# Kernel optimization log

Hardware: AMD Instinct MI355X
Metric: run time of the kernel (lower is better)

Reference implementation:

```python
import jax, jax.numpy as jnp
import numpy as np

NUM_GROUPS = 19  # cityscapes classes; groups in the grouped conv
GATES = 4
SLABS = 4  # hidden slabs per class


def setup_inputs() -> dict:
    key = jax.random.key(0)
    k1, k2, k3, k4, k5 = jax.random.split(key, 5)
    B, H, Wd = 4, 256, 512
    x = jax.random.normal(k1, (B, NUM_GROUPS, H, Wd), dtype=jnp.float32)
    h = jax.random.normal(k2, (B, NUM_GROUPS, SLABS, H, Wd), dtype=jnp.float32)
    c = jax.random.normal(k3, (B, NUM_GROUPS, SLABS, H, Wd), dtype=jnp.float32)
    # Conv2d(95 -> 304, k=3, groups=19): weight (304, 5, 3, 3), bias (304,)
    fan_in = 5 * 3 * 3
    bound = 1.0 / np.sqrt(fan_in)
    W = jax.random.uniform(k4, (4 * NUM_GROUPS * SLABS, 5, 3, 3), minval=-bound, maxval=bound, dtype=jnp.float32)
    b = jax.random.uniform(k5, (4 * NUM_GROUPS * SLABS,), minval=-bound, maxval=bound, dtype=jnp.float32)
    return {"x": x, "h": h, "c": c, "W": W, "b": b}


def reference(x, h, c, W, b):
    B, _, H, Wd = x.shape
    # Strided interleave: channel g*5+0 = x[:,g], g*5+1..4 = h[:,g,0..3]
    xh = jnp.concatenate([x[:, :, None], h], axis=2).reshape(B, NUM_GROUPS * 5, H, Wd)
    A = jax.lax.conv_general_dilated(
        xh, W, window_strides=(1, 1), padding=[(1, 1), (1, 1)],
        feature_group_count=NUM_GROUPS,
        dimension_numbers=("NCHW", "OIHW", "NCHW"))
    A = A + b[None, :, None, None]
    A = A.reshape(B, NUM_GROUPS, GATES, SLABS, H, Wd)
    i = jax.nn.sigmoid(A[:, :, 0])
    f = jax.nn.sigmoid(A[:, :, 1])
    o = jax.nn.sigmoid(A[:, :, 2])
    g = jnp.tanh(A[:, :, 3])
    new_c = f * c + i * g
    new_h = o * jnp.tanh(new_c)
    return (new_h, new_c)
```

## Files before the change

### kernel.cpp

```cpp
#include <hip/hip_runtime.h>
#include <hip/hip_bf16.h>

#define NG      19
#define HEIGHT  256
#define WIDTH   512
#define HW      (HEIGHT*WIDTH)
#define BATCH   4
#define TH      16
#define TW      64
#define HALO_R  18
#define HALO_CU 34
#define CH_U32  (HALO_R*HALO_CU)
#define LDS_U32 (5*CH_U32)
#define WFRAG_SHORTS (NG*64*16)
#define BIAS_FLOATS (NG*16)

typedef __attribute__((ext_vector_type(8))) short short8;
typedef __attribute__((ext_vector_type(4))) float f32x4;
typedef __attribute__((ext_vector_type(4))) unsigned int u32x4;

static __device__ __forceinline__ unsigned int bfbits(float f) {
    return (unsigned int)__builtin_bit_cast(unsigned short, __float2bfloat16(f));
}
static __device__ __forceinline__ unsigned int fsh16(unsigned int hi, unsigned int lo) {
    return (unsigned int)((((unsigned long long)hi << 32) | lo) >> 16);
}
__device__ __forceinline__ float fsigmoid(float x) {
    return __builtin_amdgcn_rcpf(1.0f + __builtin_amdgcn_exp2f(-1.44269504f * x));
}
__device__ __forceinline__ float ftanh(float x) {
    return 2.0f * __builtin_amdgcn_rcpf(1.0f + __builtin_amdgcn_exp2f(-2.88539008f * x)) - 1.0f;
}

__global__ void wxform_kernel(const float* __restrict__ W,
                              const float* __restrict__ b,
                              short* __restrict__ wdst,
                              float* __restrict__ bdst) {
    int i = blockIdx.x * 256 + threadIdx.x;
    if (i < WFRAG_SHORTS) {
        int g   = i / 1024;
        int r   = i & 1023;
        int l   = r >> 4;
        int j   = r & 15;
        int q   = l >> 4;
        int row = l & 15;
        int s    = row >> 2;
        int gate = row & 3;
        int half = j >> 3;
        int jj   = j & 7;
        int m  = 8*half + 2*q + (jj >> 2);
        int kc = jj & 3;
        float wv = 0.0f;
        if (m <= 14 && kc < 3) {
            int ic = m / 3, kr = m % 3;
            int oc = g*16 + gate*4 + s;
            wv = W[((oc*5 + ic)*3 + kr)*3 + kc];
        }
        wdst[i] = (short)__builtin_bit_cast(unsigned short, __float2bfloat16(wv));
    } else if (i < WFRAG_SHORTS + BIAS_FLOATS) {
        int idx = i - WFRAG_SHORTS;
        int g = idx >> 4;
        int r = idx & 15;
        int s = r >> 2, gate = r & 3;
        bdst[idx] = b[g*16 + gate*4 + s];
    }
}

__launch_bounds__(256, 4)
__global__ void convlstm_mfma(const float* __restrict__ x,
                              const float* __restrict__ h,
                              const float* __restrict__ c,
                              const short* __restrict__ wfrag,
                              const float* __restrict__ biasp,
                              float* __restrict__ out) {
    __shared__ unsigned int lds[LDS_U32];

    const int t    = threadIdx.x;
    const int bid  = blockIdx.x;
    const int bg   = bid >> 7;
    const int tile = bid & 127;
    const int tr0  = (tile >> 3) * TH;
    const int tc0  = (tile & 7)  * TW;
    const int g    = bg % NG;

    const int w  = t >> 6;
    const int l  = t & 63;
    const int q  = l >> 4;
    const int li = l & 15;

    const int NC_OFF   = BATCH * NG * 4 * HW;
    const int rowbase0 = (bg*4 + q)*HW + (tr0 + w*4)*WIDTH + tc0 + 4*li;
    f32x4 cp[4];
    #pragma unroll
    for (int tr4 = 0; tr4 < 4; ++tr4)
        cp[tr4] = __builtin_nontemporal_load(
            reinterpret_cast<const f32x4*>(c + rowbase0 + tr4*WIDTH));

    const short8* ap = reinterpret_cast<const short8*>(wfrag + (g*64 + l)*16);
    const short8 a_lo = ap[0];
    const short8 a_hi = ap[1];
    f32x4 bias4;
    {
        float4 bv = *reinterpret_cast<const float4*>(biasp + g*16 + q*4);
        bias4[0] = bv.x; bias4[1] = bv.y; bias4[2] = bv.z; bias4[3] = bv.w;
    }

    const float* xb = x + bg * HW;
    const float* hb = h + (bg * 4) * HW;
    for (int p = t; p < LDS_U32; p += 256) {
        int ch  = p / CH_U32;  int rem = p - ch * CH_U32;
        int r   = rem / HALO_CU;
        int j   = rem - r * HALO_CU;
        int gr  = tr0 + r - 1;
        int gc  = tc0 + 2*j - 1;
        const float* base = (ch == 0) ? xb : hb + (ch - 1) * HW;
        float v0 = 0.0f, v1 = 0.0f;
        if (gr >= 0 && gr < HEIGHT) {
            const float* rowp = base + gr * WIDTH;
            if (gc >= 0 && gc < WIDTH) v0 = rowp[gc];
            if (gc + 1 < WIDTH)        v1 = rowp[gc + 1];
        }
        lds[p] = bfbits(v0) | (bfbits(v1) << 16);
    }
    __syncthreads();

    int cbase[4];
    #pragma unroll
    for (int i = 0; i < 4; ++i) {
        int m = (i < 2) ? (2*q + i) : (8 + 2*q + (i - 2));
        if (m > 14) m = 14;
        cbase[i] = (m/3)*(CH_U32*4) + (m%3)*(HALO_CU*4) + 8*li;
    }
    const char* ldsb = reinterpret_cast<const char*>(lds);

    #pragma unroll
    for (int tr4 = 0; tr4 < 4; ++tr4) {
        const int tr = w*4 + tr4;
        uint2 dv[4][2];
        #pragma unroll
        for (int i = 0; i < 4; ++i) {
            const uint2* pp = reinterpret_cast<const uint2*>(
                ldsb + cbase[i] + tr * (HALO_CU*4));
            dv[i][0] = pp[0];
            dv[i][1] = pp[1];
        }
        float nh4[4], nc4[4];
        #pragma unroll
        for (int n = 0; n < 4; ++n) {
            u32x4 blo_u, bhi_u;
            #pragma unroll
            for (int i = 0; i < 4; ++i) {
                const unsigned int d0 = dv[i][0].x, d1 = dv[i][0].y;
                const unsigned int d2 = dv[i][1].x, d3 = dv[i][1].y;
                unsigned int w0, w1;
                if (n == 0)      { w0 = d0;           w1 = d1;           }
                else if (n == 1) { w0 = fsh16(d1,d0); w1 = fsh16(d2,d1); }
                else if (n == 2) { w0 = d1;           w1 = d2;           }
                else             { w0 = fsh16(d2,d1); w1 = fsh16(d3,d2); }
                if (i < 2) { blo_u[2*i]     = w0; blo_u[2*i+1]     = w1; }
                else       { bhi_u[2*(i-2)] = w0; bhi_u[2*(i-2)+1] = w1; }
            }
            const short8 blo = __builtin_bit_cast(short8, blo_u);
            const short8 bhi = __builtin_bit_cast(short8, bhi_u);

            f32x4 acc = bias4;
            acc = __builtin_amdgcn_mfma_f32_16x16x32_bf16(a_lo, blo, acc, 0, 0, 0);
            acc = __builtin_amdgcn_mfma_f32_16x16x32_bf16(a_hi, bhi, acc, 0, 0, 0);

            const float cv = cp[tr4][n];
            const float iv = fsigmoid(acc[0]);
            const float fv = fsigmoid(acc[1]);
            const float ov = fsigmoid(acc[2]);
            const float gv = ftanh   (acc[3]);
            const float nc = fv * cv + iv * gv;
            nc4[n] = nc;
            nh4[n] = ov * ftanh(nc);
        }
        const int rowchan = rowbase0 + tr4*WIDTH;
        f32x4 nhv; nhv[0]=nh4[0]; nhv[1]=nh4[1]; nhv[2]=nh4[2]; nhv[3]=nh4[3];
        f32x4 ncv; ncv[0]=nc4[0]; ncv[1]=nc4[1]; ncv[2]=nc4[2]; ncv[3]=nc4[3];
        __builtin_nontemporal_store(nhv, reinterpret_cast<f32x4*>(out + rowchan));
        __builtin_nontemporal_store(ncv, reinterpret_cast<f32x4*>(out + NC_OFF + rowchan));
    }
}

extern "C" void kernel_launch(void* const* d_in, const int* in_sizes, int n_in,
                              void* d_out, int out_size, void* d_ws, size_t ws_size,
                              hipStream_t stream) {
    (void)in_sizes; (void)n_in; (void)out_size; (void)ws_size;
    const float* x = (const float*)d_in[0];
    const float* h = (const float*)d_in[1];
    const float* c = (const float*)d_in[2];
    const float* W = (const float*)d_in[3];
    const float* b = (const float*)d_in[4];
    float* out = (float*)d_out;

    short* wdst = (short*)d_ws;
    float* bdst = (float*)((char*)d_ws + WFRAG_SHORTS * sizeof(short));

    hipLaunchKernelGGL(wxform_kernel,
                       dim3((WFRAG_SHORTS + BIAS_FLOATS + 255) / 256), dim3(256),
                       0, stream, W, b, wdst, bdst);
    hipLaunchKernelGGL(convlstm_mfma, dim3(BATCH * NG * 128), dim3(256),
                       0, stream, x, h, c, (const short*)wdst, bdst, out);
}
```

Before: 146.5 us.

## Fold gate scales into weights, dual-shifted LDS layout, vectorized halo loads, merged reciprocals

Prescales the weights and bias by -log2(e) (or -2log2(e) for the g gate) so that the gate nonlinearities become bare exp2 calls. The sigmoid and tanh reciprocals are then merged algebraically into two rcp operations per output. The halo fill now issues vectorized float2 global loads and stores two LDS copies offset by one bf16 element, which removes the 16-bit funnel shifts in the inner loop. The c loads are also software-pipelined one row ahead. In exchange, LDS use doubles, which may lower occupancy, and the merged reciprocals slightly change numerical behavior for large exponents.

```diff
diff --git a/kernel.cpp b/kernel.cpp
--- a/kernel.cpp
+++ b/kernel.cpp
@@ -12,24 +12,21 @@
 #define HALO_CU 34
 #define CH_U32  (HALO_R*HALO_CU)
 #define LDS_U32 (5*CH_U32)
+#define ROWB    (HALO_CU*4)
+#define CHB     (CH_U32*4)
 #define WFRAG_SHORTS (NG*64*16)
-#define BIAS_FLOATS (NG*16)
+#define BIAS_FLOATS  (NG*16)
 
 typedef __attribute__((ext_vector_type(8))) short short8;
 typedef __attribute__((ext_vector_type(4))) float f32x4;
+typedef __attribute__((ext_vector_type(2))) float f32x2;
 typedef __attribute__((ext_vector_type(4))) unsigned int u32x4;
 
 static __device__ __forceinline__ unsigned int bfbits(float f) {
     return (unsigned int)__builtin_bit_cast(unsigned short, __float2bfloat16(f));
 }
-static __device__ __forceinline__ unsigned int fsh16(unsigned int hi, unsigned int lo) {
-    return (unsigned int)((((unsigned long long)hi << 32) | lo) >> 16);
-}
-__device__ __forceinline__ float fsigmoid(float x) {
-    return __builtin_amdgcn_rcpf(1.0f + __builtin_amdgcn_exp2f(-1.44269504f * x));
-}
-__device__ __forceinline__ float ftanh(float x) {
-    return 2.0f * __builtin_amdgcn_rcpf(1.0f + __builtin_amdgcn_exp2f(-2.88539008f * x)) - 1.0f;
+static __device__ __forceinline__ unsigned int pack2(float lo, float hi) {
+    return bfbits(lo) | (bfbits(hi) << 16);
 }
 
 __global__ void wxform_kernel(const float* __restrict__ W,
@@ -54,7 +51,8 @@
         if (m <= 14 && kc < 3) {
             int ic = m / 3, kr = m % 3;
             int oc = g*16 + gate*4 + s;
-            wv = W[((oc*5 + ic)*3 + kr)*3 + kc];
+            float scale = (gate == 3) ? -2.88539008f : -1.44269504f;
+            wv = scale * W[((oc*5 + ic)*3 + kr)*3 + kc];
         }
         wdst[i] = (short)__builtin_bit_cast(unsigned short, __float2bfloat16(wv));
     } else if (i < WFRAG_SHORTS + BIAS_FLOATS) {
@@ -62,7 +60,8 @@
         int g = idx >> 4;
         int r = idx & 15;
         int s = r >> 2, gate = r & 3;
-        bdst[idx] = b[g*16 + gate*4 + s];
+        float scale = (gate == 3) ? -2.88539008f : -1.44269504f;
+        bdst[idx] = scale * b[g*16 + gate*4 + s];
     }
 }
 
@@ -73,15 +72,16 @@
                               const short* __restrict__ wfrag,
                               const float* __restrict__ biasp,
                               float* __restrict__ out) {
-    __shared__ unsigned int lds[LDS_U32];
-
-    const int t    = threadIdx.x;
-    const int bid  = blockIdx.x;
-    const int bg   = bid >> 7;
-    const int tile = bid & 127;
-    const int tr0  = (tile >> 3) * TH;
-    const int tc0  = (tile & 7)  * TW;
-    const int g    = bg % NG;
+    __shared__ unsigned int lds0[LDS_U32];
+    __shared__ unsigned int lds1[LDS_U32];
+
+    const int t     = threadIdx.x;
+    const int bid   = blockIdx.x;
+    const int plane = bid >> 7;
+    const int tile  = bid & 127;
+    const int tr0   = (tile >> 3) * TH;
+    const int tc0   = (tile & 7)  * TW;
+    const int g     = plane % NG;
 
     const int w  = t >> 6;
     const int l  = t & 63;
@@ -89,76 +89,95 @@
     const int li = l & 15;
 
     const int NC_OFF   = BATCH * NG * 4 * HW;
-    const int rowbase0 = (bg*4 + q)*HW + (tr0 + w*4)*WIDTH + tc0 + 4*li;
-    f32x4 cp[4];
-    #pragma unroll
-    for (int tr4 = 0; tr4 < 4; ++tr4)
-        cp[tr4] = __builtin_nontemporal_load(
-            reinterpret_cast<const f32x4*>(c + rowbase0 + tr4*WIDTH));
+    const int rowbase0 = (plane*4 + q)*HW + (tr0 + w*4)*WIDTH + tc0 + 4*li;
+
+    f32x4 cvrow = __builtin_nontemporal_load(
+        reinterpret_cast<const f32x4*>(c + rowbase0));
 
     const short8* ap = reinterpret_cast<const short8*>(wfrag + (g*64 + l)*16);
     const short8 a_lo = ap[0];
     const short8 a_hi = ap[1];
-    f32x4 bias4;
-    {
-        float4 bv = *reinterpret_cast<const float4*>(biasp + g*16 + q*4);
-        bias4[0] = bv.x; bias4[1] = bv.y; bias4[2] = bv.z; bias4[3] = bv.w;
-    }
-
-    const float* xb = x + bg * HW;
-    const float* hb = h + (bg * 4) * HW;
-    for (int p = t; p < LDS_U32; p += 256) {
-        int ch  = p / CH_U32;  int rem = p - ch * CH_U32;
-        int r   = rem / HALO_CU;
-        int j   = rem - r * HALO_CU;
-        int gr  = tr0 + r - 1;
-        int gc  = tc0 + 2*j - 1;
-        const float* base = (ch == 0) ? xb : hb + (ch - 1) * HW;
-        float v0 = 0.0f, v1 = 0.0f;
-        if (gr >= 0 && gr < HEIGHT) {
-            const float* rowp = base + gr * WIDTH;
-            if (gc >= 0 && gc < WIDTH) v0 = rowp[gc];
-            if (gc + 1 < WIDTH)        v1 = rowp[gc + 1];
-        }
-        lds[p] = bfbits(v0) | (bfbits(v1) << 16);
-    }
-    __syncthreads();
-
-    int cbase[4];
+    const f32x4 bias4 = *reinterpret_cast<const f32x4*>(biasp + g*16 + q*4);
+
+    const float* xb = x + plane * HW;
+    const float* hb = h + (plane * 4) * HW;
+    const bool lt = (tc0 == 0), rt = (tc0 == 448);
+
+    int r  = t / HALO_CU;
+    int j2 = t - r * HALO_CU;
+    int ch = 0;
+
+    #pragma unroll
+    for (int half = 0; half < 2; ++half) {
+        f32x2 pf[6]; float ex[6]; int pidx[6]; bool vld[6];
+        #pragma unroll
+        for (int k2 = 0; k2 < 6; ++k2) {
+            const int k = half*6 + k2;
+            const int p = t + 256*k;
+            const bool v = (k < 11) ? true : (p < LDS_U32);
+            pidx[k2] = p;  vld[k2] = v;
+            const int  gr  = tr0 + r - 1;
+            const bool rok = v && ((unsigned)gr < HEIGHT);
+            const bool pok = rok && !(lt && j2 == 0) && !(rt && j2 == 33);
+            const bool eok = rok && !(rt && j2 >= 32);
+            const float* bp = (ch == 0) ? xb : (hb + (ch - 1) * HW);
+            const int off = gr*WIDTH + tc0 + 2*j2 - 2;
+            f32x2 z; z[0] = 0.0f; z[1] = 0.0f;
+            pf[k2] = pok ? *reinterpret_cast<const f32x2*>(bp + off) : z;
+            ex[k2] = eok ? bp[off + 2] : 0.0f;
+            j2 += 18; r += 7;
+            if (j2 >= HALO_CU) { j2 -= HALO_CU; r += 1; }
+            if (r  >= HALO_R)  { r  -= HALO_R;  ch += 1; }
+        }
+        #pragma unroll
+        for (int k2 = 0; k2 < 6; ++k2) {
+            if (vld[k2]) {
+                lds0[pidx[k2]] = pack2(pf[k2][0], pf[k2][1]);
+                lds1[pidx[k2]] = pack2(pf[k2][1], ex[k2]);
+            }
+        }
+    }
+
+    asm volatile("s_waitcnt lgkmcnt(0)" ::: "memory");
+    __builtin_amdgcn_s_barrier();
+    asm volatile("" ::: "memory");
+
+    int dbase[4];
     #pragma unroll
     for (int i = 0; i < 4; ++i) {
         int m = (i < 2) ? (2*q + i) : (8 + 2*q + (i - 2));
         if (m > 14) m = 14;
-        cbase[i] = (m/3)*(CH_U32*4) + (m%3)*(HALO_CU*4) + 8*li;
-    }
-    const char* ldsb = reinterpret_cast<const char*>(lds);
+        dbase[i] = ((m/3)*CHB + (m%3)*ROWB + 8*li) >> 2;
+    }
 
     #pragma unroll
     for (int tr4 = 0; tr4 < 4; ++tr4) {
-        const int tr = w*4 + tr4;
-        uint2 dv[4][2];
-        #pragma unroll
-        for (int i = 0; i < 4; ++i) {
-            const uint2* pp = reinterpret_cast<const uint2*>(
-                ldsb + cbase[i] + tr * (HALO_CU*4));
-            dv[i][0] = pp[0];
-            dv[i][1] = pp[1];
-        }
+        f32x4 cvnext = cvrow;
+        if (tr4 < 3)
+            cvnext = __builtin_nontemporal_load(
+                reinterpret_cast<const f32x4*>(c + rowbase0 + (tr4+1)*WIDTH));
+
+        const int tr  = w*4 + tr4;
+        const int drw = tr * (ROWB >> 2);
+        const int d0 = dbase[0] + drw, d1 = dbase[1] + drw;
+        const int d2 = dbase[2] + drw, d3 = dbase[3] + drw;
+
         float nh4[4], nc4[4];
         #pragma unroll
         for (int n = 0; n < 4; ++n) {
             u32x4 blo_u, bhi_u;
-            #pragma unroll
-            for (int i = 0; i < 4; ++i) {
-                const unsigned int d0 = dv[i][0].x, d1 = dv[i][0].y;
-                const unsigned int d2 = dv[i][1].x, d3 = dv[i][1].y;
-                unsigned int w0, w1;
-                if (n == 0)      { w0 = d0;           w1 = d1;           }
-                else if (n == 1) { w0 = fsh16(d1,d0); w1 = fsh16(d2,d1); }
-                else if (n == 2) { w0 = d1;           w1 = d2;           }
-                else             { w0 = fsh16(d2,d1); w1 = fsh16(d3,d2); }
-                if (i < 2) { blo_u[2*i]     = w0; blo_u[2*i+1]     = w1; }
-                else       { bhi_u[2*(i-2)] = w0; bhi_u[2*(i-2)+1] = w1; }
+            if (n == 0) {
+                blo_u[0]=lds1[d0];   blo_u[1]=lds1[d0+1]; blo_u[2]=lds1[d1];   blo_u[3]=lds1[d1+1];
+                bhi_u[0]=lds1[d2];   bhi_u[1]=lds1[d2+1]; bhi_u[2]=lds1[d3];   bhi_u[3]=lds1[d3+1];
+            } else if (n == 1) {
+                blo_u[0]=lds0[d0+1]; blo_u[1]=lds0[d0+2]; blo_u[2]=lds0[d1+1]; blo_u[3]=lds0[d1+2];
+                bhi_u[0]=lds0[d2+1]; bhi_u[1]=lds0[d2+2]; bhi_u[2]=lds0[d3+1]; bhi_u[3]=lds0[d3+2];
+            } else if (n == 2) {
+                blo_u[0]=lds1[d0+1]; blo_u[1]=lds1[d0+2]; blo_u[2]=lds1[d1+1]; blo_u[3]=lds1[d1+2];
+                bhi_u[0]=lds1[d2+1]; bhi_u[1]=lds1[d2+2]; bhi_u[2]=lds1[d3+1]; bhi_u[3]=lds1[d3+2];
+            } else {
+                blo_u[0]=lds0[d0+2]; blo_u[1]=lds0[d0+3]; blo_u[2]=lds0[d1+2]; blo_u[3]=lds0[d1+3];
+                bhi_u[0]=lds0[d2+2]; bhi_u[1]=lds0[d2+3]; bhi_u[2]=lds0[d3+2]; bhi_u[3]=lds0[d3+3];
             }
             const short8 blo = __builtin_bit_cast(short8, blo_u);
             const short8 bhi = __builtin_bit_cast(short8, bhi_u);
@@ -167,20 +186,28 @@
             acc = __builtin_amdgcn_mfma_f32_16x16x32_bf16(a_lo, blo, acc, 0, 0, 0);
             acc = __builtin_amdgcn_mfma_f32_16x16x32_bf16(a_hi, bhi, acc, 0, 0, 0);
 
-            const float cv = cp[tr4][n];
-            const float iv = fsigmoid(acc[0]);
-            const float fv = fsigmoid(acc[1]);
-            const float ov = fsigmoid(acc[2]);
-            const float gv = ftanh   (acc[3]);
-            const float nc = fv * cv + iv * gv;
+            const float cv = cvrow[n];
+            const float u  = __builtin_amdgcn_exp2f(acc[0]);
+            const float v  = __builtin_amdgcn_exp2f(acc[1]);
+            const float wo = __builtin_amdgcn_exp2f(acc[2]);
+            const float z  = __builtin_amdgcn_exp2f(acc[3]);
+            const float pu = 1.0f + u,  pv = 1.0f + v;
+            const float pw = 1.0f + wo, pz = 1.0f + z;
+            const float puz = pu * pz;
+            const float r1  = __builtin_amdgcn_rcpf(pv * puz);
+            const float nc  = fmaf(cv, puz, (1.0f - z) * pv) * r1;
+            const float tt2 = __builtin_amdgcn_exp2f(-2.88539008f * nc);
+            const float r2  = __builtin_amdgcn_rcpf(pw * (1.0f + tt2));
             nc4[n] = nc;
-            nh4[n] = ov * ftanh(nc);
-        }
+            nh4[n] = (1.0f - tt2) * r2;
+        }
+
         const int rowchan = rowbase0 + tr4*WIDTH;
         f32x4 nhv; nhv[0]=nh4[0]; nhv[1]=nh4[1]; nhv[2]=nh4[2]; nhv[3]=nh4[3];
         f32x4 ncv; ncv[0]=nc4[0]; ncv[1]=nc4[1]; ncv[2]=nc4[2]; ncv[3]=nc4[3];
         __builtin_nontemporal_store(nhv, reinterpret_cast<f32x4*>(out + rowchan));
         __builtin_nontemporal_store(ncv, reinterpret_cast<f32x4*>(out + NC_OFF + rowchan));
+        cvrow = cvnext;
     }
 }
 
```

New measurement: 144.2 us. Within noise of the previous version (-1.6%).
